# Kernel optimization log

Measured on AMD Instinct MI355X. Metric: run time of the kernel, lower is better.

The kernel has to match this reference:

```python
import jax, jax.numpy as jnp
import numpy as np

NUM_EMBEDDINGS = 1024
EMBEDDING_DIM = 64
COMMITMENT_COST = 0.25
DECAY = 0.99
EPS = 1e-5


def setup_inputs() -> dict:
    key = jax.random.key(0)
    k1, k2, k3 = jax.random.split(key, 3)
    z = jax.random.normal(k1, (64, EMBEDDING_DIM, 32, 32), dtype=jnp.float32)
    embedding = jax.random.normal(k2, (NUM_EMBEDDINGS, EMBEDDING_DIM), dtype=jnp.float32)
    cluster_size = jnp.zeros((NUM_EMBEDDINGS,), dtype=jnp.float32)
    ema_w = jax.random.normal(k3, (NUM_EMBEDDINGS, EMBEDDING_DIM), dtype=jnp.float32)
    return {"z": z, "embedding": embedding, "cluster_size": cluster_size, "ema_w": ema_w}


def reference(z, embedding, cluster_size, ema_w):
    B, D, H, W = z.shape
    K = embedding.shape[0]
    # (B, H, W, D) -> (N, D)
    z_flat = jnp.transpose(z, (0, 2, 3, 1)).reshape(-1, D)
    # squared L2 distances to every code: (N, K)
    d = (jnp.sum(z_flat * z_flat, axis=1, keepdims=True)
         + jnp.sum(embedding * embedding, axis=1)
         - 2.0 * z_flat @ embedding.T)
    indices = jnp.argmin(d, axis=1)  # (N,)
    z_q = embedding[indices].reshape(B, H, W, D).transpose(0, 3, 1, 2)

    # EMA codebook update (training branch); no gradients flow here in torch (.data ops)
    zf = jax.lax.stop_gradient(z_flat)
    counts = jax.ops.segment_sum(jnp.ones_like(zf[:, 0]), indices, num_segments=K)
    dw = jax.ops.segment_sum(zf, indices, num_segments=K)  # encodings.T @ z_flat
    new_cluster_size = DECAY * cluster_size + (1.0 - DECAY) * counts
    new_ema_w = DECAY * ema_w + (1.0 - DECAY) * dw
    n = jnp.sum(new_cluster_size)
    cs = (new_cluster_size + EPS) / (n + K * EPS) * n
    new_embedding = new_ema_w / cs[:, None]

    loss = COMMITMENT_COST * jnp.mean((z - jax.lax.stop_gradient(z_q)) ** 2)
    z_q_st = z + jax.lax.stop_gradient(z_q - z)  # straight-through
    return (z_q_st, loss, indices.reshape(B, H, W), new_cluster_size, new_ema_w, new_embedding)
```

## Files before the change

kernel.cpp:

```cpp
#include <hip/hip_runtime.h>
#include <stdint.h>

typedef unsigned short ushort;
typedef __attribute__((ext_vector_type(8)))  short bfrag;
typedef __attribute__((ext_vector_type(16))) float f32x16;

#define D      64
#define K      1024
#define HW     1024
#define NROWS  65536
#define NELEM  (NROWS * D)
#define BAND   0.01f

#define O_ZQ   0
#define O_LOSS 4194304
#define O_IDX  4194305
#define O_NCS  4259841
#define O_EMAW 4260865
#define O_EMB  4326401

#define WB_EH     0x00000
#define WB_EL     0x20000
#define WB_ESQ    0x40000
#define WB_OFFS   0x41000
#define WB_CURSOR 0x42000
#define WB_COUNTS 0x43000
#define WB_LOSSN  0x44000
#define WB_RLIST  0x45000

__device__ __forceinline__ unsigned bf16r(float x) {
    unsigned u = __float_as_uint(x);
    return (u + 0x7FFFu + ((u >> 16) & 1u)) >> 16;
}
__device__ __forceinline__ float bf16f(unsigned h) {
    return __uint_as_float(h << 16);
}

__global__ __launch_bounds__(64) void vq_prep_e(
    const float* __restrict__ emb, ushort* __restrict__ eh,
    ushort* __restrict__ el, float* __restrict__ esq)
{
    const int k = blockIdx.x;
    const int d = threadIdx.x;
    float v = emb[k * 64 + d];
    unsigned hh = bf16r(v);
    float rem = v - bf16f(hh);
    eh[k * 64 + d] = (ushort)hh;
    el[k * 64 + d] = (ushort)bf16r(rem);
    float a = v * v;
#pragma unroll
    for (int off = 32; off; off >>= 1) a += __shfl_xor(a, off);
    if (d == 0) esq[k] = a;
}

__global__ __launch_bounds__(256, 2) void vq_dist_kernel(
    const float* __restrict__ z, const short* __restrict__ eh_g,
    const short* __restrict__ el_g, const float* __restrict__ esq_g,
    float* __restrict__ out, unsigned* __restrict__ counts,
    unsigned* __restrict__ rcnt, int* __restrict__ rlist)
{
    __shared__ __align__(16) short zh_lds[128 * 64];
    __shared__ __align__(16) short zl_lds[128 * 64];
    __shared__ __align__(16) short eh_lds[2][64 * 64];
    __shared__ __align__(16) short el_lds[2][64 * 64];
    __shared__ float esq_lds[1024];

    const int tid  = threadIdx.x;
    const int lane = tid & 63;
    const int wave = tid >> 6;
    const int col  = lane & 31;
    const int h    = lane >> 5;
    const int n0   = blockIdx.x * 128;
    const int b    = n0 >> 10;
    const int hw0  = n0 & 1023;

    for (int it = 0; it < 4; ++it) {
        int task = it * 256 + tid;
        int row  = task & 127;
        int kq   = task >> 7;
        const float* zp = z + (size_t)b * 65536 + (size_t)(kq * 8) * 1024 + hw0 + row;
        bfrag vh, vl;
#pragma unroll
        for (int m = 0; m < 8; ++m) {
            float t = -2.0f * zp[m * 1024];
            unsigned hh = bf16r(t);
            float rem = t - bf16f(hh);
            vh[m] = (short)hh;
            vl[m] = (short)bf16r(rem);
        }
        int unit = kq ^ (row & 7);
        *(bfrag*)&zh_lds[row * 64 + unit * 8] = vh;
        *(bfrag*)&zl_lds[row * 64 + unit * 8] = vl;
    }
    for (int it = 0; it < 4; ++it) {
        int t = it * 256 + tid;
        esq_lds[t] = esq_g[t];
    }

    bfrag pfh[2], pfl[2];
    auto loadE = [&](int cb) {
#pragma unroll
        for (int q = 0; q < 2; ++q) {
            int u = q * 256 + tid;
            int code = u >> 3, m = u & 7;
            pfh[q] = *(const bfrag*)&eh_g[(size_t)(cb + code) * 64 + m * 8];
            pfl[q] = *(const bfrag*)&el_g[(size_t)(cb + code) * 64 + m * 8];
        }
    };
    auto writeE = [&](int buf) {
#pragma unroll
        for (int q = 0; q < 2; ++q) {
            int u = q * 256 + tid;
            int code = u >> 3, m = u & 7;
            int unit = ((code >> 5) * 4 + (m >> 1)) * 64 +
                       ((((m & 1) << 5) | (code & 31)) ^ (m & 7));
            *(bfrag*)&eh_lds[buf][unit * 8] = pfh[q];
            *(bfrag*)&el_lds[buf][unit * 8] = pfl[q];
        }
    };

    loadE(0);
    writeE(0);
    loadE(64);
    __syncthreads();

    const int wrow = wave * 32 + col;
    bfrag zhA[4], zlA[4];
#pragma unroll
    for (int j = 0; j < 4; ++j) {
        int kq = j * 2 + h;
        int unit = kq ^ (wrow & 7);
        zhA[j] = *(const bfrag*)&zh_lds[wrow * 64 + unit * 8];
        zlA[j] = *(const bfrag*)&zl_lds[wrow * 64 + unit * 8];
    }

    float t1s[16], t2s[16];
    unsigned t1c[16];
#pragma unroll
    for (int i = 0; i < 16; ++i) { t1s[i] = INFINITY; t2s[i] = INFINITY; t1c[i] = 0; }

    for (int ch = 0; ch < 16; ++ch) {
        const int cb  = ch * 64;
        const int buf = ch & 1;

#pragma unroll
        for (int t = 0; t < 2; ++t) {
            const int ccode = cb + t * 32 + col;
            const float esqv = esq_lds[ccode];
            bfrag ehB[4], elB[4];
#pragma unroll
            for (int j = 0; j < 4; ++j) {
                int m = j * 2 + h;
                int unit = (t * 4 + j) * 64 + (((h << 5) | col) ^ (m & 7));
                ehB[j] = *(const bfrag*)&eh_lds[buf][unit * 8];
                elB[j] = *(const bfrag*)&el_lds[buf][unit * 8];
            }
            f32x16 acc;
#pragma unroll
            for (int i = 0; i < 16; ++i) acc[i] = esqv;
#pragma unroll
            for (int j = 0; j < 4; ++j)
                acc = __builtin_amdgcn_mfma_f32_32x32x16_bf16(zhA[j], ehB[j], acc, 0, 0, 0);
#pragma unroll
            for (int j = 0; j < 4; ++j)
                acc = __builtin_amdgcn_mfma_f32_32x32x16_bf16(zhA[j], elB[j], acc, 0, 0, 0);
#pragma unroll
            for (int j = 0; j < 4; ++j)
                acc = __builtin_amdgcn_mfma_f32_32x32x16_bf16(zlA[j], ehB[j], acc, 0, 0, 0);

#pragma unroll
            for (int i = 0; i < 16; ++i) {
                float s = acc[i];
                t2s[i] = __builtin_amdgcn_fmed3f(t1s[i], t2s[i], s);
                bool lt = s < t1s[i];
                t1s[i] = fminf(t1s[i], s);
                t1c[i] = lt ? (unsigned)ccode : t1c[i];
            }
        }

        if (ch < 15) {
            writeE(buf ^ 1);
            if (ch < 14) loadE(cb + 128);
        }
        __syncthreads();
    }

#pragma unroll
    for (int i = 0; i < 16; ++i) {
        float v = t1s[i], w = t2s[i];
        int   c = (int)t1c[i];
#pragma unroll
        for (int m = 1; m < 32; m <<= 1) {
            float ov = __shfl_xor(v, m);
            int   oc = __shfl_xor(c, m);
            float ow = __shfl_xor(w, m);
            float mx = fmaxf(v, ov);
            w = fminf(fminf(w, ow), mx);
            bool take = (ov < v) || (ov == v && oc < c);
            v = take ? ov : v;
            c = take ? oc : c;
        }
        if ((lane & 31) == 0) {
            int row = (i & 3) + ((i >> 2) << 3) + (h << 2);
            int n = n0 + wave * 32 + row;
            out[O_IDX + n] = (float)c;
            atomicAdd(&counts[c], 1u);
            if (w - v < BAND) {
                unsigned p = atomicAdd(rcnt, 1u);
                rlist[p] = n;
            }
        }
    }
}

__global__ __launch_bounds__(256) void vq_rescore(
    const float* __restrict__ z, const float* __restrict__ emb,
    const float* __restrict__ esq, const unsigned* __restrict__ rcnt,
    const int* __restrict__ rlist, float* __restrict__ out,
    unsigned* __restrict__ counts)
{
    __shared__ float zrow[64];
    __shared__ float rs[4];
    __shared__ int   rc[4];
    const int tid = threadIdx.x;
    const unsigned cnt = rcnt[0];

    for (unsigned i = blockIdx.x; i < cnt; i += gridDim.x) {
        const int n = rlist[i];
        const int b = n >> 10, hw = n & 1023;
        __syncthreads();
        if (tid < 64) zrow[tid] = z[(size_t)b * 65536 + (size_t)tid * 1024 + hw];
        __syncthreads();

        float best = INFINITY; int bc = 0;
        for (int rep = 0; rep < 4; ++rep) {
            int code = rep * 256 + tid;
            const float4* er = (const float4*)(emb + (size_t)code * 64);
            float a0 = 0.f, a1 = 0.f, a2 = 0.f, a3 = 0.f;
#pragma unroll
            for (int q = 0; q < 16; ++q) {
                float4 e = er[q];
                a0 = fmaf(zrow[q * 4 + 0], e.x, a0);
                a1 = fmaf(zrow[q * 4 + 1], e.y, a1);
                a2 = fmaf(zrow[q * 4 + 2], e.z, a2);
                a3 = fmaf(zrow[q * 4 + 3], e.w, a3);
            }
            float s = fmaf(-2.f, (a0 + a1) + (a2 + a3), esq[code]);
            if (s < best || (s == best && code < bc)) { best = s; bc = code; }
        }
        for (int m = 1; m < 64; m <<= 1) {
            float ov = __shfl_xor(best, m);
            int   oc = __shfl_xor(bc, m);
            bool take = (ov < best) || (ov == best && oc < bc);
            best = take ? ov : best;
            bc   = take ? oc : bc;
        }
        if ((tid & 63) == 0) { rs[tid >> 6] = best; rc[tid >> 6] = bc; }
        __syncthreads();
        if (tid == 0) {
            float fb = rs[0]; int fc = rc[0];
#pragma unroll
            for (int q = 1; q < 4; ++q) {
                bool take = (rs[q] < fb) || (rs[q] == fb && rc[q] < fc);
                fb = take ? rs[q] : fb;
                fc = take ? rc[q] : fc;
            }
            int old = (int)out[O_IDX + n];
            if (fc != old) {
                atomicAdd(&counts[old], (unsigned)-1);
                atomicAdd(&counts[fc], 1u);
                out[O_IDX + n] = (float)fc;
            }
        }
    }
}

__global__ __launch_bounds__(1024) void vq_scan_kernel(
    const unsigned* __restrict__ counts, const float* __restrict__ cs,
    unsigned* __restrict__ offs, unsigned* __restrict__ cursor,
    float* __restrict__ out, float* __restrict__ n_val)
{
    __shared__ unsigned wtot[16], wbase[16];
    __shared__ float    fred[16];
    const int k    = threadIdx.x;
    const int lane = k & 63;
    const int w    = k >> 6;

    unsigned c = counts[k];
    unsigned v = c;
#pragma unroll
    for (int off = 1; off < 64; off <<= 1) {
        unsigned t = __shfl_up(v, off);
        if (lane >= off) v += t;
    }
    if (lane == 63) wtot[w] = v;

    float ncs = 0.99f * cs[k] + 0.01f * (float)c;
    out[O_NCS + k] = ncs;
    float s = ncs;
#pragma unroll
    for (int off = 32; off; off >>= 1) s += __shfl_down(s, off);
    if (lane == 0) fred[w] = s;

    __syncthreads();
    if (k == 0) {
        unsigned base = 0;
        float nt = 0.f;
#pragma unroll
        for (int i = 0; i < 16; ++i) {
            wbase[i] = base;
            base += wtot[i];
            nt += fred[i];
        }
        n_val[0] = nt;
    }
    __syncthreads();
    unsigned o = wbase[w] + (v - c);
    offs[k]   = o;
    cursor[k] = o;
}

__global__ __launch_bounds__(256) void vq_scatter_kernel(
    const float* __restrict__ z, const float* __restrict__ emb,
    float* __restrict__ out, unsigned* __restrict__ cursor,
    float* __restrict__ loss_acc)
{
    const int tid = threadIdx.x;
    const int n   = blockIdx.x * 256 + tid;
    const int b   = n >> 10;
    const int hw  = n & 1023;
    const int k   = (int)out[O_IDX + n];

    const unsigned pos = atomicAdd(&cursor[k], 1u);
    const float*  zb  = z + (size_t)b * 65536 + hw;
    const float4* ek4 = (const float4*)emb + (size_t)k * 16;
    float* dst = out + O_ZQ + (size_t)pos * 64;

    float lacc = 0.f;
#pragma unroll
    for (int i = 0; i < 16; ++i) {
        float4 e = ek4[i];
        float z0 = zb[(i * 4 + 0) * 1024];
        float z1 = zb[(i * 4 + 1) * 1024];
        float z2 = zb[(i * 4 + 2) * 1024];
        float z3 = zb[(i * 4 + 3) * 1024];
        *(float4*)&dst[i * 4] = make_float4(z0, z1, z2, z3);
        float d0 = z0 - e.x, d1 = z1 - e.y, d2 = z2 - e.z, d3 = z3 - e.w;
        lacc = fmaf(d0, d0, lacc);
        lacc = fmaf(d1, d1, lacc);
        lacc = fmaf(d2, d2, lacc);
        lacc = fmaf(d3, d3, lacc);
    }

    for (int off = 32; off; off >>= 1) lacc += __shfl_down(lacc, off);
    if ((tid & 63) == 0) atomicAdd(loss_acc, lacc);
}

__global__ __launch_bounds__(256) void vq_upd_kernel(
    const float* __restrict__ zf, const unsigned* __restrict__ offs,
    const unsigned* __restrict__ counts, const float* __restrict__ ema_w,
    const float* __restrict__ n_val, const float* __restrict__ loss_acc,
    float* __restrict__ out)
{
    __shared__ float red[4][64];
    const int k   = blockIdx.x;
    const int tid = threadIdx.x;
    const int d   = tid & 63;
    const int q   = tid >> 6;
    const unsigned off = offs[k];
    const unsigned cnt = counts[k];

    float acc = 0.f;
    unsigned j = q;
    for (; j + 12 < cnt; j += 16) {
        float v0 = zf[(size_t)(off + j)      * 64 + d];
        float v1 = zf[(size_t)(off + j + 4)  * 64 + d];
        float v2 = zf[(size_t)(off + j + 8)  * 64 + d];
        float v3 = zf[(size_t)(off + j + 12) * 64 + d];
        acc += v0; acc += v1; acc += v2; acc += v3;
    }
    for (; j < cnt; j += 4) acc += zf[(size_t)(off + j) * 64 + d];

    red[q][d] = acc;
    __syncthreads();
    if (q == 0) {
        float dw = red[0][d] + red[1][d] + red[2][d] + red[3][d];
        float nw = 0.99f * ema_w[k * 64 + d] + 0.01f * dw;
        out[O_EMAW + k * 64 + d] = nw;
        float n   = n_val[0];
        float ncs = out[O_NCS + k];
        float csv = (ncs + 1e-5f) / (n + 1024e-5f) * n;
        out[O_EMB + k * 64 + d] = nw / csv;
    }
    if (k == 0 && tid == 0)
        out[O_LOSS] = 0.25f * loss_acc[0] / (float)NELEM;
}

__global__ __launch_bounds__(256) void vq_zqwrite_kernel(
    const float* __restrict__ z, const float* __restrict__ emb,
    float* __restrict__ out)
{
    const int tid = threadIdx.x;
    const int n   = blockIdx.x * 128 + (tid & 127);
    const int h   = tid >> 7;
    const int b   = n >> 10;
    const int hw  = n & 1023;
    const int k   = (int)out[O_IDX + n];

    const float*  zb  = z   + ((size_t)(b * D + h * 32)) * HW + hw;
    float*        oq  = out + O_ZQ + ((size_t)(b * D + h * 32)) * HW + hw;
    const float4* ek4 = (const float4*)emb + (size_t)k * 16 + h * 8;

#pragma unroll
    for (int i = 0; i < 8; ++i) {
        float4 e = ek4[i];
        float z0 = zb[(i * 4 + 0) * HW];
        float z1 = zb[(i * 4 + 1) * HW];
        float z2 = zb[(i * 4 + 2) * HW];
        float z3 = zb[(i * 4 + 3) * HW];
        oq[(i * 4 + 0) * HW] = z0 + (e.x - z0);
        oq[(i * 4 + 1) * HW] = z1 + (e.y - z1);
        oq[(i * 4 + 2) * HW] = z2 + (e.z - z2);
        oq[(i * 4 + 3) * HW] = z3 + (e.w - z3);
    }
}

extern "C" void kernel_launch(void* const* d_in, const int* in_sizes, int n_in,
                              void* d_out, int out_size, void* d_ws, size_t ws_size,
                              hipStream_t stream) {
    const float* z     = (const float*)d_in[0];
    const float* emb   = (const float*)d_in[1];
    const float* cs    = (const float*)d_in[2];
    const float* ema_w = (const float*)d_in[3];
    float* out = (float*)d_out;

    char* W = (char*)d_ws;
    short*    eh_g   = (short*)(W + WB_EH);
    short*    el_g   = (short*)(W + WB_EL);
    float*    esq    = (float*)(W + WB_ESQ);
    unsigned* offs   = (unsigned*)(W + WB_OFFS);
    unsigned* cursor = (unsigned*)(W + WB_CURSOR);
    unsigned* counts = (unsigned*)(W + WB_COUNTS);
    float*    lossa  = (float*)(W + WB_LOSSN);
    float*    n_val  = lossa + 1;
    unsigned* rcnt   = (unsigned*)(W + WB_LOSSN + 8);
    int*      rlist  = (int*)(W + WB_RLIST);

    hipMemsetAsync(W + WB_COUNTS, 0, 0x2000, stream);

    vq_prep_e<<<1024, 64, 0, stream>>>(emb, (ushort*)eh_g, (ushort*)el_g, esq);
    vq_dist_kernel<<<512, 256, 0, stream>>>(z, eh_g, el_g, esq, out, counts,
                                            rcnt, rlist);
    vq_rescore<<<512, 256, 0, stream>>>(z, emb, esq, rcnt, rlist, out, counts);
    vq_scan_kernel<<<1, 1024, 0, stream>>>(counts, cs, offs, cursor, out, n_val);
    vq_scatter_kernel<<<256, 256, 0, stream>>>(z, emb, out, cursor, lossa);
    vq_upd_kernel<<<1024, 256, 0, stream>>>(out + O_ZQ, offs, counts, ema_w,
                                            n_val, lossa, out);
    vq_zqwrite_kernel<<<512, 256, 0, stream>>>(z, emb, out);
}
```

Measured before the change: 219.7 us.

## Fuse z_q write into scatter, interleave MFMA chains, drop memset launch

```diff
diff --git a/kernel.cpp b/kernel.cpp
--- a/kernel.cpp
+++ b/kernel.cpp
@@ -27,6 +27,8 @@
 #define WB_COUNTS 0x43000
 #define WB_LOSSN  0x44000
 #define WB_RLIST  0x45000
+#define WB_ZF     0x100000
+#define WS_NEED_FUSED (0x100000 + 0x1000000)
 
 __device__ __forceinline__ unsigned bf16r(float x) {
     unsigned u = __float_as_uint(x);
@@ -36,12 +38,18 @@
     return __uint_as_float(h << 16);
 }
 
-__global__ __launch_bounds__(64) void vq_prep_e(
+__global__ __launch_bounds__(256) void vq_prep_e(
     const float* __restrict__ emb, ushort* __restrict__ eh,
-    ushort* __restrict__ el, float* __restrict__ esq)
-{
-    const int k = blockIdx.x;
-    const int d = threadIdx.x;
+    ushort* __restrict__ el, float* __restrict__ esq,
+    unsigned* __restrict__ zero_region)
+{
+    const int tid = threadIdx.x;
+    if (blockIdx.x == 0) {
+#pragma unroll
+        for (int i = 0; i < 8; ++i) zero_region[i * 256 + tid] = 0u;
+    }
+    const int k = blockIdx.x * 4 + (tid >> 6);
+    const int d = tid & 63;
     float v = emb[k * 64 + d];
     unsigned hh = bf16r(v);
     float rem = v - bf16f(hh);
@@ -143,44 +151,60 @@
         const int cb  = ch * 64;
         const int buf = ch & 1;
 
-#pragma unroll
-        for (int t = 0; t < 2; ++t) {
-            const int ccode = cb + t * 32 + col;
-            const float esqv = esq_lds[ccode];
-            bfrag ehB[4], elB[4];
-#pragma unroll
-            for (int j = 0; j < 4; ++j) {
-                int m = j * 2 + h;
-                int unit = (t * 4 + j) * 64 + (((h << 5) | col) ^ (m & 7));
-                ehB[j] = *(const bfrag*)&eh_lds[buf][unit * 8];
-                elB[j] = *(const bfrag*)&el_lds[buf][unit * 8];
-            }
-            f32x16 acc;
-#pragma unroll
-            for (int i = 0; i < 16; ++i) acc[i] = esqv;
-#pragma unroll
-            for (int j = 0; j < 4; ++j)
-                acc = __builtin_amdgcn_mfma_f32_32x32x16_bf16(zhA[j], ehB[j], acc, 0, 0, 0);
-#pragma unroll
-            for (int j = 0; j < 4; ++j)
-                acc = __builtin_amdgcn_mfma_f32_32x32x16_bf16(zhA[j], elB[j], acc, 0, 0, 0);
-#pragma unroll
-            for (int j = 0; j < 4; ++j)
-                acc = __builtin_amdgcn_mfma_f32_32x32x16_bf16(zlA[j], ehB[j], acc, 0, 0, 0);
-
-#pragma unroll
-            for (int i = 0; i < 16; ++i) {
-                float s = acc[i];
-                t2s[i] = __builtin_amdgcn_fmed3f(t1s[i], t2s[i], s);
-                bool lt = s < t1s[i];
-                t1s[i] = fminf(t1s[i], s);
-                t1c[i] = lt ? (unsigned)ccode : t1c[i];
-            }
-        }
+        bfrag ehB0[4], elB0[4], ehB1[4], elB1[4];
+#pragma unroll
+        for (int j = 0; j < 4; ++j) {
+            int m = j * 2 + h;
+            int sw = (((h << 5) | col) ^ (m & 7));
+            ehB0[j] = *(const bfrag*)&eh_lds[buf][(j * 64 + sw) * 8];
+            elB0[j] = *(const bfrag*)&el_lds[buf][(j * 64 + sw) * 8];
+            ehB1[j] = *(const bfrag*)&eh_lds[buf][((4 + j) * 64 + sw) * 8];
+            elB1[j] = *(const bfrag*)&el_lds[buf][((4 + j) * 64 + sw) * 8];
+        }
+        const float esq0 = esq_lds[cb + col];
+        const float esq1 = esq_lds[cb + 32 + col];
+        const unsigned c0 = cb + col;
+        const unsigned c1 = cb + 32 + col;
+
+        f32x16 acc0, acc1;
+#pragma unroll
+        for (int i = 0; i < 16; ++i) { acc0[i] = esq0; acc1[i] = esq1; }
+
+        __builtin_amdgcn_s_setprio(1);
+#pragma unroll
+        for (int j = 0; j < 4; ++j) {
+            acc0 = __builtin_amdgcn_mfma_f32_32x32x16_bf16(zhA[j], ehB0[j], acc0, 0, 0, 0);
+            acc1 = __builtin_amdgcn_mfma_f32_32x32x16_bf16(zhA[j], ehB1[j], acc1, 0, 0, 0);
+        }
+#pragma unroll
+        for (int j = 0; j < 4; ++j) {
+            acc0 = __builtin_amdgcn_mfma_f32_32x32x16_bf16(zhA[j], elB0[j], acc0, 0, 0, 0);
+            acc1 = __builtin_amdgcn_mfma_f32_32x32x16_bf16(zhA[j], elB1[j], acc1, 0, 0, 0);
+        }
+#pragma unroll
+        for (int j = 0; j < 4; ++j) {
+            acc0 = __builtin_amdgcn_mfma_f32_32x32x16_bf16(zlA[j], ehB0[j], acc0, 0, 0, 0);
+            acc1 = __builtin_amdgcn_mfma_f32_32x32x16_bf16(zlA[j], ehB1[j], acc1, 0, 0, 0);
+        }
+        __builtin_amdgcn_s_setprio(0);
 
         if (ch < 15) {
             writeE(buf ^ 1);
             if (ch < 14) loadE(cb + 128);
+        }
+
+#pragma unroll
+        for (int i = 0; i < 16; ++i) {
+            float s0 = acc0[i];
+            t2s[i] = __builtin_amdgcn_fmed3f(t1s[i], t2s[i], s0);
+            bool lt0 = s0 < t1s[i];
+            t1s[i] = fminf(t1s[i], s0);
+            t1c[i] = lt0 ? c0 : t1c[i];
+            float s1 = acc1[i];
+            t2s[i] = __builtin_amdgcn_fmed3f(t1s[i], t2s[i], s1);
+            bool lt1 = s1 < t1s[i];
+            t1s[i] = fminf(t1s[i], s1);
+            t1c[i] = lt1 ? c1 : t1c[i];
         }
         __syncthreads();
     }
@@ -320,7 +344,48 @@
     cursor[k] = o;
 }
 
-__global__ __launch_bounds__(256) void vq_scatter_kernel(
+__global__ __launch_bounds__(256) void vq_scatter_fused(
+    const float* __restrict__ z, const float* __restrict__ emb,
+    float* __restrict__ out, float* __restrict__ zf,
+    unsigned* __restrict__ cursor, float* __restrict__ loss_acc)
+{
+    const int tid = threadIdx.x;
+    const int n   = blockIdx.x * 256 + tid;
+    const int b   = n >> 10;
+    const int hw  = n & 1023;
+    const int k   = (int)out[O_IDX + n];
+
+    const unsigned pos = atomicAdd(&cursor[k], 1u);
+    const float*  zb  = z   + (size_t)b * 65536 + hw;
+    float*        oq  = out + O_ZQ + (size_t)b * 65536 + hw;
+    const float4* ek4 = (const float4*)emb + (size_t)k * 16;
+    float* dst = zf + (size_t)pos * 64;
+
+    float lacc = 0.f;
+#pragma unroll
+    for (int i = 0; i < 16; ++i) {
+        float4 e = ek4[i];
+        float z0 = zb[(i * 4 + 0) * 1024];
+        float z1 = zb[(i * 4 + 1) * 1024];
+        float z2 = zb[(i * 4 + 2) * 1024];
+        float z3 = zb[(i * 4 + 3) * 1024];
+        *(float4*)&dst[i * 4] = make_float4(z0, z1, z2, z3);
+        oq[(i * 4 + 0) * 1024] = z0 + (e.x - z0);
+        oq[(i * 4 + 1) * 1024] = z1 + (e.y - z1);
+        oq[(i * 4 + 2) * 1024] = z2 + (e.z - z2);
+        oq[(i * 4 + 3) * 1024] = z3 + (e.w - z3);
+        float d0 = z0 - e.x, d1 = z1 - e.y, d2 = z2 - e.z, d3 = z3 - e.w;
+        lacc = fmaf(d0, d0, lacc);
+        lacc = fmaf(d1, d1, lacc);
+        lacc = fmaf(d2, d2, lacc);
+        lacc = fmaf(d3, d3, lacc);
+    }
+
+    for (int off = 32; off; off >>= 1) lacc += __shfl_down(lacc, off);
+    if ((tid & 63) == 0) atomicAdd(loss_acc, lacc);
+}
+
+__global__ __launch_bounds__(256) void vq_scatter_sep(
     const float* __restrict__ z, const float* __restrict__ emb,
     float* __restrict__ out, unsigned* __restrict__ cursor,
     float* __restrict__ loss_acc)
@@ -445,16 +510,24 @@
     float*    n_val  = lossa + 1;
     unsigned* rcnt   = (unsigned*)(W + WB_LOSSN + 8);
     int*      rlist  = (int*)(W + WB_RLIST);
-
-    hipMemsetAsync(W + WB_COUNTS, 0, 0x2000, stream);
-
-    vq_prep_e<<<1024, 64, 0, stream>>>(emb, (ushort*)eh_g, (ushort*)el_g, esq);
+    float*    zf     = (float*)(W + WB_ZF);
+
+    const bool fused = ws_size >= (size_t)WS_NEED_FUSED;
+
+    vq_prep_e<<<256, 256, 0, stream>>>(emb, (ushort*)eh_g, (ushort*)el_g, esq,
+                                       counts);
     vq_dist_kernel<<<512, 256, 0, stream>>>(z, eh_g, el_g, esq, out, counts,
                                             rcnt, rlist);
-    vq_rescore<<<512, 256, 0, stream>>>(z, emb, esq, rcnt, rlist, out, counts);
+    vq_rescore<<<128, 256, 0, stream>>>(z, emb, esq, rcnt, rlist, out, counts);
     vq_scan_kernel<<<1, 1024, 0, stream>>>(counts, cs, offs, cursor, out, n_val);
-    vq_scatter_kernel<<<256, 256, 0, stream>>>(z, emb, out, cursor, lossa);
-    vq_upd_kernel<<<1024, 256, 0, stream>>>(out + O_ZQ, offs, counts, ema_w,
-                                            n_val, lossa, out);
-    vq_zqwrite_kernel<<<512, 256, 0, stream>>>(z, emb, out);
-}
+    if (fused) {
+        vq_scatter_fused<<<256, 256, 0, stream>>>(z, emb, out, zf, cursor, lossa);
+        vq_upd_kernel<<<1024, 256, 0, stream>>>(zf, offs, counts, ema_w,
+                                                n_val, lossa, out);
+    } else {
+        vq_scatter_sep<<<256, 256, 0, stream>>>(z, emb, out, cursor, lossa);
+        vq_upd_kernel<<<1024, 256, 0, stream>>>(out + O_ZQ, offs, counts, ema_w,
+                                                n_val, lossa, out);
+        vq_zqwrite_kernel<<<512, 256, 0, stream>>>(z, emb, out);
+    }
+}
```

Result: no change. 218.5 us (-0.6%).
